# Kernel optimization log

Measured on AMD Instinct MI355X. Metric: run time of the kernel, lower is better.

The kernel has to match this reference:

```python
import jax, jax.numpy as jnp
import numpy as np

B, IN, OUT, LUT_SIZE = 32, 8192, 16384, 256


def setup_inputs() -> dict:
    key = jax.random.key(0)
    k1, k2, k3 = jax.random.split(key, 3)
    x = jax.random.normal(k1, (B, IN), dtype=jnp.float32)
    # int8 weight codes, stored as indices in [0, 256) into the dequant LUT
    weight_idx = jax.random.randint(k2, (OUT, IN), 0, LUT_SIZE, dtype=jnp.int32)
    # symmetric uniform dequant levels: code c -> (c - 128) * scale
    scale = jnp.float32(0.05 / 128.0)
    lut = (jnp.arange(LUT_SIZE, dtype=jnp.float32) - 128.0) * scale  # [256]
    bias = jax.random.normal(k3, (OUT,), dtype=jnp.float32) * 0.02
    return {"x": x, "lut": lut, "bias": bias, "weight_idx": weight_idx}


def reference(x, lut, bias, weight_idx):
    # LUT dequantization: gather fp32 weight values from the 256-entry table
    W = lut[weight_idx]                      # [OUT, IN] fp32
    # y = x @ W^T + b   (einsum: b=batch tokens, i=in_features, o=out_features)
    return jnp.einsum("bi,oi->bo", x, W) + bias  # [B, OUT]
```

## Files before the change

### kernel.cpp

```cpp
#include <hip/hip_runtime.h>

#define IN_F   8192
#define OUT_F  16384
#define BATCH  32
#define KBLKS  2
#define NWAVE  4
#define KSLICE (IN_F / KBLKS / NWAVE)

typedef __attribute__((ext_vector_type(8))) short  bf16x8;
typedef __attribute__((ext_vector_type(4))) float  f32x4;

__device__ __forceinline__ unsigned f2bf(float f) {
    unsigned u = __builtin_bit_cast(unsigned, f);
    return (u + 0x7fffu + ((u >> 16) & 1u)) >> 16;
}

__device__ __forceinline__ unsigned pk_i2bf(int a, int b) {
    unsigned fa = __builtin_bit_cast(unsigned, (float)a);
    unsigned fb = __builtin_bit_cast(unsigned, (float)b);
#if __has_builtin(__builtin_amdgcn_perm)
    return __builtin_amdgcn_perm(fb, fa, 0x07060302u);
#else
    return (fa >> 16) | (fb & 0xffff0000u);
#endif
}

__global__ __launch_bounds__(256) void prep_kernel(
        const float* __restrict__ x, const float* __restrict__ lut,
        unsigned short* __restrict__ xbf, float* __restrict__ sumx) {
    const int b = blockIdx.x;
    const int t = threadIdx.x;
    const float s = lut[129];
    const float4* xr = (const float4*)(x + b * IN_F);
    ushort4* xo = (ushort4*)(xbf + b * IN_F);
    float acc = 0.f;
    #pragma unroll
    for (int i = 0; i < IN_F / 4 / 256; ++i) {
        float4 v = xr[t + i * 256];
        acc += v.x + v.y + v.z + v.w;
        ushort4 o;
        o.x = (unsigned short)f2bf(v.x * s);
        o.y = (unsigned short)f2bf(v.y * s);
        o.z = (unsigned short)f2bf(v.z * s);
        o.w = (unsigned short)f2bf(v.w * s);
        xo[t + i * 256] = o;
    }
    __shared__ float red[256];
    red[t] = acc;
    __syncthreads();
    for (int off = 128; off > 0; off >>= 1) {
        if (t < off) red[t] += red[t + off];
        __syncthreads();
    }
    if (t == 0) sumx[b] = red[0];
}

__global__ __launch_bounds__(256) void init_kernel(
        const float* __restrict__ bias, const float* __restrict__ lut,
        const float* __restrict__ sumx, float* __restrict__ out) {
    int i = blockIdx.x * 256 + threadIdx.x;
    int b = i >> 12;
    float corr = lut[0] * sumx[b];
    const float4* b4 = (const float4*)bias;
    float4 v = b4[i & 4095];
    v.x += corr; v.y += corr; v.z += corr; v.w += corr;
    ((float4*)out)[i] = v;
}

__global__ __launch_bounds__(256, 8) void gemm_kernel(
        const unsigned short* __restrict__ xbf,
        const int* __restrict__ widx,
        float* __restrict__ out) {
    const int tid   = threadIdx.x;
    const int wave  = tid >> 6;
    const int lane  = tid & 63;
    const int col16 = lane & 15;
    const int quad  = lane >> 4;
    const int ntile = blockIdx.x >> 1;
    const int kblk  = blockIdx.x & 1;
    const int n     = ntile * 16 + col16;
    const int k0    = (kblk * NWAVE + wave) * KSLICE + quad * 8;

    const int* wp = widx + (long)n * IN_F + k0;
    const unsigned short* xp0 = xbf + col16 * IN_F + k0;
    const unsigned short* xp1 = xp0 + 16 * IN_F;

    f32x4 acc0 = {0.f, 0.f, 0.f, 0.f};
    f32x4 acc1 = {0.f, 0.f, 0.f, 0.f};

    #pragma unroll 2
    for (int kk = 0; kk < KSLICE; kk += 32) {
        int4   c0 = *(const int4*)(wp + kk);
        int4   c1 = *(const int4*)(wp + kk + 4);
        bf16x8 a0 = *(const bf16x8*)(xp0 + kk);
        bf16x8 a1 = *(const bf16x8*)(xp1 + kk);

        union { unsigned u[4]; bf16x8 v; } bB;
        bB.u[0] = pk_i2bf(c0.x, c0.y);
        bB.u[1] = pk_i2bf(c0.z, c0.w);
        bB.u[2] = pk_i2bf(c1.x, c1.y);
        bB.u[3] = pk_i2bf(c1.z, c1.w);
        acc0 = __builtin_amdgcn_mfma_f32_16x16x32_bf16(a0, bB.v, acc0, 0, 0, 0);
        acc1 = __builtin_amdgcn_mfma_f32_16x16x32_bf16(a1, bB.v, acc1, 0, 0, 0);
    }

    const int row = quad * 4;
    float* op = out + (long)ntile * 16 + col16;
    #pragma unroll
    for (int r = 0; r < 4; ++r) {
        unsafeAtomicAdd(op + (long)(row + r) * OUT_F,      acc0[r]);
        unsafeAtomicAdd(op + (long)(row + r + 16) * OUT_F, acc1[r]);
    }
}

extern "C" void kernel_launch(void* const* d_in, const int* in_sizes, int n_in,
                              void* d_out, int out_size, void* d_ws, size_t ws_size,
                              hipStream_t stream) {
    const float* x    = (const float*)d_in[0];
    const float* lut  = (const float*)d_in[1];
    const float* bias = (const float*)d_in[2];
    const int*   widx = (const int*)d_in[3];
    float* out = (float*)d_out;

    unsigned short* xbf = (unsigned short*)d_ws;
    float* sumx = (float*)((char*)d_ws + BATCH * IN_F * 2);

    prep_kernel<<<BATCH, 256, 0, stream>>>(x, lut, xbf, sumx);
    init_kernel<<<(BATCH * OUT_F / 4) / 256, 256, 0, stream>>>(bias, lut, sumx, out);
    gemm_kernel<<<OUT_F / 16 * KBLKS, 256, 0, stream>>>(xbf, widx, out);
}
```

Measured before the change: 712.2 us.

## Stage weight-index tiles through LDS via async global_load_lds and drop atomics

The GEMM now stages 16-row by 512-column tiles of int32 weight codes into padded LDS using direct global-to-LDS async copies, so each wave's global reads become fully coalesced 1KB rows instead of strided 32-byte per-lane chunks. The K split across blocks is removed, and each block reduces its four waves' partial accumulators in LDS and writes the output directly, with bias and zero-point correction fused in. This removes the init kernel and all float atomics. In exchange, there are half as many blocks, the loop has no double-buffering (a full vmcnt(0) wait plus a barrier every tile), and the launch bound drops to 4 blocks per CU.

New measurement: 700.2 us. No clear change (-1.7%).

```diff
diff --git a/kernel.cpp b/kernel.cpp
--- a/kernel.cpp
+++ b/kernel.cpp
@@ -3,9 +3,9 @@
 #define IN_F   8192
 #define OUT_F  16384
 #define BATCH  32
-#define KBLKS  2
-#define NWAVE  4
-#define KSLICE (IN_F / KBLKS / NWAVE)
+#define KT     512
+#define NTILES (IN_F / KT)
+#define PITCH  2064
 
 typedef __attribute__((ext_vector_type(8))) short  bf16x8;
 typedef __attribute__((ext_vector_type(4))) float  f32x4;
@@ -23,6 +23,13 @@
 #else
     return (fa >> 16) | (fb & 0xffff0000u);
 #endif
+}
+
+__device__ __forceinline__ void async_copy16(const int* g, void* l) {
+    __builtin_amdgcn_global_load_lds(
+        (const __attribute__((address_space(1))) unsigned*)g,
+        (__attribute__((address_space(3))) unsigned*)l,
+        16, 0, 0);
 }
 
 __global__ __launch_bounds__(256) void prep_kernel(
@@ -55,61 +62,73 @@
     if (t == 0) sumx[b] = red[0];
 }
 
-__global__ __launch_bounds__(256) void init_kernel(
-        const float* __restrict__ bias, const float* __restrict__ lut,
-        const float* __restrict__ sumx, float* __restrict__ out) {
-    int i = blockIdx.x * 256 + threadIdx.x;
-    int b = i >> 12;
-    float corr = lut[0] * sumx[b];
-    const float4* b4 = (const float4*)bias;
-    float4 v = b4[i & 4095];
-    v.x += corr; v.y += corr; v.z += corr; v.w += corr;
-    ((float4*)out)[i] = v;
-}
-
-__global__ __launch_bounds__(256, 8) void gemm_kernel(
+__global__ __launch_bounds__(256, 4) void gemm_kernel(
         const unsigned short* __restrict__ xbf,
         const int* __restrict__ widx,
+        const float* __restrict__ bias,
+        const float* __restrict__ lut,
+        const float* __restrict__ sumx,
         float* __restrict__ out) {
+    __shared__ char ltile[16 * PITCH];
     const int tid   = threadIdx.x;
     const int wave  = tid >> 6;
     const int lane  = tid & 63;
     const int col16 = lane & 15;
     const int quad  = lane >> 4;
-    const int ntile = blockIdx.x >> 1;
-    const int kblk  = blockIdx.x & 1;
-    const int n     = ntile * 16 + col16;
-    const int k0    = (kblk * NWAVE + wave) * KSLICE + quad * 8;
+    const int n0    = blockIdx.x * 16;
 
-    const int* wp = widx + (long)n * IN_F + k0;
-    const unsigned short* xp0 = xbf + col16 * IN_F + k0;
+    const unsigned short* xp0 = xbf + col16 * IN_F + quad * 8;
     const unsigned short* xp1 = xp0 + 16 * IN_F;
 
     f32x4 acc0 = {0.f, 0.f, 0.f, 0.f};
     f32x4 acc1 = {0.f, 0.f, 0.f, 0.f};
 
-    #pragma unroll 2
-    for (int kk = 0; kk < KSLICE; kk += 32) {
-        int4   c0 = *(const int4*)(wp + kk);
-        int4   c1 = *(const int4*)(wp + kk + 4);
-        bf16x8 a0 = *(const bf16x8*)(xp0 + kk);
-        bf16x8 a1 = *(const bf16x8*)(xp1 + kk);
-
-        union { unsigned u[4]; bf16x8 v; } bB;
-        bB.u[0] = pk_i2bf(c0.x, c0.y);
-        bB.u[1] = pk_i2bf(c0.z, c0.w);
-        bB.u[2] = pk_i2bf(c1.x, c1.y);
-        bB.u[3] = pk_i2bf(c1.z, c1.w);
-        acc0 = __builtin_amdgcn_mfma_f32_16x16x32_bf16(a0, bB.v, acc0, 0, 0, 0);
-        acc1 = __builtin_amdgcn_mfma_f32_16x16x32_bf16(a1, bB.v, acc1, 0, 0, 0);
+    for (int t = 0; t < NTILES; ++t) {
+        const long kt = (long)t * KT;
+        #pragma unroll
+        for (int j = 0; j < 8; ++j) {
+            const int r = wave * 4 + (j >> 1);
+            const int h = j & 1;
+            async_copy16(widx + (long)(n0 + r) * IN_F + kt + h * 256 + lane * 4,
+                         ltile + r * PITCH + h * 1024);
+        }
+        asm volatile("s_waitcnt vmcnt(0)" ::: "memory");
+        __syncthreads();
+        #pragma unroll
+        for (int s = 0; s < 4; ++s) {
+            const char* bb = ltile + col16 * PITCH + wave * 512 + s * 128 + quad * 32;
+            int4 c0 = *(const int4*)(bb);
+            int4 c1 = *(const int4*)(bb + 16);
+            const long ka = kt + wave * 128 + s * 32;
+            bf16x8 a0 = *(const bf16x8*)(xp0 + ka);
+            bf16x8 a1 = *(const bf16x8*)(xp1 + ka);
+            union { unsigned u[4]; bf16x8 v; } bB;
+            bB.u[0] = pk_i2bf(c0.x, c0.y);
+            bB.u[1] = pk_i2bf(c0.z, c0.w);
+            bB.u[2] = pk_i2bf(c1.x, c1.y);
+            bB.u[3] = pk_i2bf(c1.z, c1.w);
+            acc0 = __builtin_amdgcn_mfma_f32_16x16x32_bf16(a0, bB.v, acc0, 0, 0, 0);
+            acc1 = __builtin_amdgcn_mfma_f32_16x16x32_bf16(a1, bB.v, acc1, 0, 0, 0);
+        }
+        __syncthreads();
     }
 
-    const int row = quad * 4;
-    float* op = out + (long)ntile * 16 + col16;
+    float* red = (float*)ltile;
     #pragma unroll
     for (int r = 0; r < 4; ++r) {
-        unsafeAtomicAdd(op + (long)(row + r) * OUT_F,      acc0[r]);
-        unsafeAtomicAdd(op + (long)(row + r + 16) * OUT_F, acc1[r]);
+        red[wave * 512 + (quad * 4 + r)      * 16 + col16] = acc0[r];
+        red[wave * 512 + (quad * 4 + r + 16) * 16 + col16] = acc1[r];
+    }
+    __syncthreads();
+    const float l0 = lut[0];
+    #pragma unroll
+    for (int e0 = 0; e0 < 2; ++e0) {
+        const int e = tid + e0 * 256;
+        float v = red[e] + red[e + 512] + red[e + 1024] + red[e + 1536];
+        const int m  = e >> 4;
+        const int nn = e & 15;
+        v += bias[n0 + nn] + l0 * sumx[m];
+        out[(long)m * OUT_F + n0 + nn] = v;
     }
 }
 
@@ -126,6 +145,5 @@
     float* sumx = (float*)((char*)d_ws + BATCH * IN_F * 2);
 
     prep_kernel<<<BATCH, 256, 0, stream>>>(x, lut, xbf, sumx);
-    init_kernel<<<(BATCH * OUT_F / 4) / 256, 256, 0, stream>>>(bias, lut, sumx, out);
-    gemm_kernel<<<OUT_F / 16 * KBLKS, 256, 0, stream>>>(xbf, widx, out);
+    gemm_kernel<<<OUT_F / 16, 256, 0, stream>>>(xbf, widx, bias, lut, sumx, out);
 }
```
